# Kernel tuning notes

Hardware: AMD Instinct MI355X
Metric: run time of the kernel (lower is better)

Reference implementation:

```python
import jax, jax.numpy as jnp
import numpy as np

N_WORD_IDS, N_TAG_IDS, N_DEPREL_IDS = 100000, 48, 40
N_WORD_F, N_TAG_F, N_DEPREL_F = 18, 18, 12
EMBED, HIDDEN, N_CLASSES = 128, 1024, 3
B = 16384
N_TOTAL = N_WORD_F + N_TAG_F + N_DEPREL_F  # 48


def _he(key, shape):
    fan_in = shape[0]
    return jax.random.normal(key, shape, dtype=jnp.float32) * jnp.sqrt(2.0 / fan_in)


def setup_inputs() -> dict:
    key = jax.random.key(0)
    ks = jax.random.split(key, 8)
    return {
        "word_id_batch": jax.random.randint(ks[0], (B, N_WORD_F), 0, N_WORD_IDS, dtype=jnp.int64 if jax.config.jax_enable_x64 else jnp.int32).astype(jnp.int32),
        "tag_id_batch": jax.random.randint(ks[1], (B, N_TAG_F), 0, N_TAG_IDS).astype(jnp.int32),
        "deprel_id_batch": jax.random.randint(ks[2], (B, N_DEPREL_F), 0, N_DEPREL_IDS).astype(jnp.int32),
        "word_embeddings": jax.random.normal(ks[3], (N_WORD_IDS, EMBED), dtype=jnp.float32) * 0.1,
        "tag_embeddings": _he(ks[4], (N_TAG_IDS, EMBED)),
        "deprel_embeddings": _he(ks[5], (N_DEPREL_IDS, EMBED)),
        "W_h": _he(ks[6], (N_TOTAL * EMBED, HIDDEN)),
        "b_h": jnp.zeros((HIDDEN,), jnp.float32),
        "W_o": _he(ks[7], (HIDDEN, N_CLASSES)),
        "b_o": jnp.zeros((N_CLASSES,), jnp.float32),
    }


def reference(word_id_batch, tag_id_batch, deprel_id_batch,
              word_embeddings, tag_embeddings, deprel_embeddings,
              W_h, b_h, W_o, b_o):
    # one_hot_float(ids) @ E is mathematically a row gather: E[ids]
    b = word_id_batch.shape[0]
    x = jnp.concatenate([
        word_embeddings[word_id_batch].reshape(b, -1),      # (B, 18*E)
        tag_embeddings[tag_id_batch].reshape(b, -1),        # (B, 18*E)
        deprel_embeddings[deprel_id_batch].reshape(b, -1),  # (B, 12*E)
    ], axis=1)                                              # (B, 48*E)
    h = jax.nn.relu(x @ W_h + b_h)
    # dropout is identity in eval mode (self.training == False)
    return h @ W_o + b_o
```

## Files before the change

kernel.cpp:

```cpp
#include <hip/hip_runtime.h>
#include <hip/hip_bf16.h>
#include <cstdint>

typedef unsigned short u16;
typedef __attribute__((ext_vector_type(8))) short bf16x8;
typedef __attribute__((ext_vector_type(4))) float f32x4;

#define B_ROWS 16384
#define N_HID  1024
#define K_DIM  6144
#define EMB    128
#define N_WORD 100000
#define N_TAG  48
#define N_DEP  40

__device__ __forceinline__ u16 f2bf(float x) {
  union { float f; uint32_t u; } v; v.f = x;
  uint32_t r = v.u + 0x7fffu + ((v.u >> 16) & 1u);
  return (u16)(r >> 16);
}

__device__ __forceinline__ void gload_lds16(const void* g, void* l) {
  __builtin_amdgcn_global_load_lds(
      (const __attribute__((address_space(1))) void*)g,
      (__attribute__((address_space(3))) void*)l, 16, 0, 0);
}

__global__ void init_out_kernel(float* __restrict__ out, const float* __restrict__ b_o) {
  int i = blockIdx.x * blockDim.x + threadIdx.x;
  if (i < B_ROWS * 3) out[i] = b_o[i % 3];
}

__global__ void transpose_wh_kernel(const float* __restrict__ Wh, u16* __restrict__ Wt) {
  __shared__ float tile[32][33];
  int k0 = blockIdx.x * 32, n0 = blockIdx.y * 32;
  int tx = threadIdx.x & 31, ty = threadIdx.x >> 5;
  #pragma unroll
  for (int j = 0; j < 4; ++j)
    tile[ty + j * 8][tx] = Wh[(size_t)(k0 + ty + j * 8) * N_HID + n0 + tx];
  __syncthreads();
  #pragma unroll
  for (int j = 0; j < 4; ++j)
    Wt[(size_t)(n0 + ty + j * 8) * K_DIM + k0 + tx] = f2bf(tile[tx][ty + j * 8]);
}

__global__ void cast_tables_kernel(const float* __restrict__ wordE, const float* __restrict__ tagE,
                                   const float* __restrict__ depE, u16* __restrict__ wordB,
                                   u16* __restrict__ tagB, u16* __restrict__ depB) {
  const int W8 = N_WORD * EMB / 8, T8 = N_TAG * EMB / 8, D8 = N_DEP * EMB / 8;
  int i = blockIdx.x * blockDim.x + threadIdx.x;
  const float* src; u16* dst; int j;
  if (i < W8)            { src = wordE; dst = wordB; j = i; }
  else if (i < W8 + T8)  { src = tagE;  dst = tagB;  j = i - W8; }
  else if (i < W8 + T8 + D8) { src = depE; dst = depB; j = i - W8 - T8; }
  else return;
  const float4* s = (const float4*)(src + (size_t)j * 8);
  float4 v0 = s[0], v1 = s[1];
  bf16x8 w;
  w[0] = (short)f2bf(v0.x); w[1] = (short)f2bf(v0.y);
  w[2] = (short)f2bf(v0.z); w[3] = (short)f2bf(v0.w);
  w[4] = (short)f2bf(v1.x); w[5] = (short)f2bf(v1.y);
  w[6] = (short)f2bf(v1.z); w[7] = (short)f2bf(v1.w);
  *(bf16x8*)(dst + (size_t)j * 8) = w;
}

__global__ __launch_bounds__(256, 4) void fused_v2_kernel(
    const int* __restrict__ word_ids, const int* __restrict__ tag_ids,
    const int* __restrict__ dep_ids,  const u16* __restrict__ wordB,
    const u16* __restrict__ tagB,     const u16* __restrict__ depB,
    const u16* __restrict__ Wt,       const float* __restrict__ b_h,
    const float* __restrict__ W_o,    float* __restrict__ out) {
  __shared__ u16 As[128 * 64];
  __shared__ u16 Bs[128 * 64];

  const int tid  = threadIdx.x;
  const int lane = tid & 63;
  const int wid  = tid >> 6;
  const int wr   = wid >> 1, wc = wid & 1;
  const int bm0  = blockIdx.y * 128;
  const int bn0  = blockIdx.x * 128;

  f32x4 acc[4][4] = {};

  for (int kt = 0; kt < K_DIM / 64; ++kt) {
    __syncthreads();
    {
      int f = kt >> 1, e0 = (kt & 1) << 6;
      const int* ids; const u16* tbl; int nf, fl;
      if (f < 18)      { ids = word_ids; tbl = wordB; nf = 18; fl = f; }
      else if (f < 36) { ids = tag_ids;  tbl = tagB;  nf = 18; fl = f - 18; }
      else             { ids = dep_ids;  tbl = depB;  nf = 12; fl = f - 36; }
      #pragma unroll
      for (int it = 0; it < 4; ++it) {
        int cidx = wid * 256 + it * 64 + lane;
        int r = cidx >> 3, c = cidx & 7;
        int id = ids[(bm0 + r) * nf + fl];
        const u16* src = tbl + (size_t)id * EMB + e0 + ((c ^ (r & 7)) << 3);
        gload_lds16(src, &As[(wid * 256 + it * 64) * 8]);
      }
    }
    #pragma unroll
    for (int it = 0; it < 4; ++it) {
      int cidx = wid * 256 + it * 64 + lane;
      int rn = cidx >> 3, c = cidx & 7;
      const u16* src = Wt + (size_t)(bn0 + rn) * K_DIM + kt * 64 + ((c ^ (rn & 7)) << 3);
      gload_lds16(src, &Bs[(wid * 256 + it * 64) * 8]);
    }
    __syncthreads();
    const int l15 = lane & 15, ca = lane >> 4;
    #pragma unroll
    for (int ks = 0; ks < 2; ++ks) {
      bf16x8 a[4], b[4];
      #pragma unroll
      for (int m = 0; m < 4; ++m) {
        int ra = wr * 64 + m * 16 + l15;
        int ch = (ca + ks * 4) ^ (ra & 7);
        a[m] = *(const bf16x8*)&As[ra * 64 + ch * 8];
      }
      #pragma unroll
      for (int n = 0; n < 4; ++n) {
        int rb = wc * 64 + n * 16 + l15;
        int ch = (ca + ks * 4) ^ (rb & 7);
        b[n] = *(const bf16x8*)&Bs[rb * 64 + ch * 8];
      }
      #pragma unroll
      for (int m = 0; m < 4; ++m)
        #pragma unroll
        for (int n = 0; n < 4; ++n)
          acc[m][n] = __builtin_amdgcn_mfma_f32_16x16x32_bf16(a[m], b[n], acc[m][n], 0, 0, 0);
    }
  }

  float bh[4], wo[4][3];
  #pragma unroll
  for (int n = 0; n < 4; ++n) {
    int j = bn0 + wc * 64 + n * 16 + (lane & 15);
    bh[n] = b_h[j];
    wo[n][0] = W_o[j * 3 + 0]; wo[n][1] = W_o[j * 3 + 1]; wo[n][2] = W_o[j * 3 + 2];
  }
  #pragma unroll
  for (int m = 0; m < 4; ++m) {
    #pragma unroll
    for (int reg = 0; reg < 4; ++reg) {
      float p0 = 0.f, p1 = 0.f, p2 = 0.f;
      #pragma unroll
      for (int n = 0; n < 4; ++n) {
        float h = acc[m][n][reg] + bh[n];
        h = fmaxf(h, 0.f);
        p0 += h * wo[n][0]; p1 += h * wo[n][1]; p2 += h * wo[n][2];
      }
      #pragma unroll
      for (int mask = 1; mask < 16; mask <<= 1) {
        p0 += __shfl_xor(p0, mask);
        p1 += __shfl_xor(p1, mask);
        p2 += __shfl_xor(p2, mask);
      }
      if ((lane & 15) == 0) {
        int row = bm0 + wr * 64 + m * 16 + ((lane >> 4) << 2) + reg;
        atomicAdd(&out[row * 3 + 0], p0);
        atomicAdd(&out[row * 3 + 1], p1);
        atomicAdd(&out[row * 3 + 2], p2);
      }
    }
  }
}

template <bool USE_WT>
__global__ __launch_bounds__(256, 2) void fused_parser_kernel(
    const int* __restrict__ word_ids, const int* __restrict__ tag_ids,
    const int* __restrict__ dep_ids,  const float* __restrict__ wordE,
    const float* __restrict__ tagE,   const float* __restrict__ depE,
    const float* __restrict__ Wh,     const u16* __restrict__ Wt,
    const float* __restrict__ b_h,    const float* __restrict__ W_o,
    float* __restrict__ out) {
  __shared__ u16 As[128 * 72];
  __shared__ u16 Bs[128 * 72];
  const int tid  = threadIdx.x;
  const int lane = tid & 63;
  const int wid  = tid >> 6;
  const int wr   = wid >> 1, wc = wid & 1;
  const int bm0  = blockIdx.y * 128;
  const int bn0  = blockIdx.x * 128;
  f32x4 acc[4][4] = {};
  const int r    = tid & 127;
  const int half = tid >> 7;

  for (int kt = 0; kt < K_DIM / 64; ++kt) {
    __syncthreads();
    {
      int f  = kt >> 1;
      int e0 = (kt & 1) << 6;
      int brow = bm0 + r;
      int id; const float* table;
      if (f < 18)      { id = word_ids[brow * 18 + f];        table = wordE; }
      else if (f < 36) { id = tag_ids[brow * 18 + (f - 18)];  table = tagE;  }
      else             { id = dep_ids[brow * 12 + (f - 36)];  table = depE;  }
      const float4* src = (const float4*)(table + (size_t)id * EMB + e0 + half * 32);
      u16* dst = &As[r * 72 + half * 32];
      #pragma unroll
      for (int j = 0; j < 4; ++j) {
        float4 v0 = src[2 * j], v1 = src[2 * j + 1];
        bf16x8 w;
        w[0] = (short)f2bf(v0.x); w[1] = (short)f2bf(v0.y);
        w[2] = (short)f2bf(v0.z); w[3] = (short)f2bf(v0.w);
        w[4] = (short)f2bf(v1.x); w[5] = (short)f2bf(v1.y);
        w[6] = (short)f2bf(v1.z); w[7] = (short)f2bf(v1.w);
        *(bf16x8*)(dst + j * 8) = w;
      }
    }
    if (USE_WT) {
      const bf16x8* src = (const bf16x8*)(Wt + (size_t)(bn0 + r) * K_DIM + kt * 64 + half * 32);
      u16* dst = &Bs[r * 72 + half * 32];
      #pragma unroll
      for (int j = 0; j < 4; ++j) *(bf16x8*)(dst + j * 8) = src[j];
    } else {
      int kk = tid >> 2, q = tid & 3;
      const float4* src = (const float4*)(Wh + (size_t)(kt * 64 + kk) * N_HID + bn0 + q * 32);
      #pragma unroll
      for (int j = 0; j < 8; ++j) {
        float4 v = src[j];
        int nb = q * 32 + j * 4;
        Bs[(nb + 0) * 72 + kk] = f2bf(v.x);
        Bs[(nb + 1) * 72 + kk] = f2bf(v.y);
        Bs[(nb + 2) * 72 + kk] = f2bf(v.z);
        Bs[(nb + 3) * 72 + kk] = f2bf(v.w);
      }
    }
    __syncthreads();
    const u16* pa = &As[(wr * 64 + (lane & 15)) * 72 + ((lane >> 4) * 8)];
    const u16* pb = &Bs[(wc * 64 + (lane & 15)) * 72 + ((lane >> 4) * 8)];
    #pragma unroll
    for (int ks = 0; ks < 2; ++ks) {
      bf16x8 a[4], b[4];
      #pragma unroll
      for (int m = 0; m < 4; ++m) a[m] = *(const bf16x8*)(pa + m * 16 * 72 + ks * 32);
      #pragma unroll
      for (int n = 0; n < 4; ++n) b[n] = *(const bf16x8*)(pb + n * 16 * 72 + ks * 32);
      #pragma unroll
      for (int m = 0; m < 4; ++m)
        #pragma unroll
        for (int n = 0; n < 4; ++n)
          acc[m][n] = __builtin_amdgcn_mfma_f32_16x16x32_bf16(a[m], b[n], acc[m][n], 0, 0, 0);
    }
  }

  float bh[4], wo[4][3];
  #pragma unroll
  for (int n = 0; n < 4; ++n) {
    int j = bn0 + wc * 64 + n * 16 + (lane & 15);
    bh[n] = b_h[j];
    wo[n][0] = W_o[j * 3 + 0]; wo[n][1] = W_o[j * 3 + 1]; wo[n][2] = W_o[j * 3 + 2];
  }
  #pragma unroll
  for (int m = 0; m < 4; ++m) {
    #pragma unroll
    for (int reg = 0; reg < 4; ++reg) {
      float p0 = 0.f, p1 = 0.f, p2 = 0.f;
      #pragma unroll
      for (int n = 0; n < 4; ++n) {
        float h = acc[m][n][reg] + bh[n];
        h = fmaxf(h, 0.f);
        p0 += h * wo[n][0]; p1 += h * wo[n][1]; p2 += h * wo[n][2];
      }
      #pragma unroll
      for (int mask = 1; mask < 16; mask <<= 1) {
        p0 += __shfl_xor(p0, mask);
        p1 += __shfl_xor(p1, mask);
        p2 += __shfl_xor(p2, mask);
      }
      if ((lane & 15) == 0) {
        int row = bm0 + wr * 64 + m * 16 + ((lane >> 4) << 2) + reg;
        atomicAdd(&out[row * 3 + 0], p0);
        atomicAdd(&out[row * 3 + 1], p1);
        atomicAdd(&out[row * 3 + 2], p2);
      }
    }
  }
}

extern "C" void kernel_launch(void* const* d_in, const int* in_sizes, int n_in,
                              void* d_out, int out_size, void* d_ws, size_t ws_size,
                              hipStream_t stream) {
  const int*   word_ids = (const int*)d_in[0];
  const int*   tag_ids  = (const int*)d_in[1];
  const int*   dep_ids  = (const int*)d_in[2];
  const float* wordE    = (const float*)d_in[3];
  const float* tagE     = (const float*)d_in[4];
  const float* depE     = (const float*)d_in[5];
  const float* Wh       = (const float*)d_in[6];
  const float* b_h      = (const float*)d_in[7];
  const float* W_o      = (const float*)d_in[8];
  const float* b_o      = (const float*)d_in[9];
  float*       out      = (float*)d_out;

  const size_t WT_ELEMS   = (size_t)N_HID * K_DIM;
  const size_t WORD_ELEMS = (size_t)N_WORD * EMB;
  const size_t TAG_ELEMS  = (size_t)N_TAG * EMB;
  const size_t DEP_ELEMS  = (size_t)N_DEP * EMB;
  const size_t NEED_V2 = (WT_ELEMS + WORD_ELEMS + TAG_ELEMS + DEP_ELEMS) * sizeof(u16);
  const size_t NEED_WT = WT_ELEMS * sizeof(u16);

  u16* Wt    = (u16*)d_ws;
  u16* wordB = Wt + WT_ELEMS;
  u16* tagB  = wordB + WORD_ELEMS;
  u16* depB  = tagB + TAG_ELEMS;

  init_out_kernel<<<(B_ROWS * 3 + 255) / 256, 256, 0, stream>>>(out, b_o);

  dim3 grid(N_HID / 128, B_ROWS / 128);
  if (d_ws && ws_size >= NEED_V2) {
    transpose_wh_kernel<<<dim3(K_DIM / 32, N_HID / 32), 256, 0, stream>>>(Wh, Wt);
    const int CAST8 = (int)((WORD_ELEMS + TAG_ELEMS + DEP_ELEMS) / 8);
    cast_tables_kernel<<<(CAST8 + 255) / 256, 256, 0, stream>>>(wordE, tagE, depE, wordB, tagB, depB);
    fused_v2_kernel<<<grid, 256, 0, stream>>>(
        word_ids, tag_ids, dep_ids, wordB, tagB, depB, Wt, b_h, W_o, out);
  } else if (d_ws && ws_size >= NEED_WT) {
    transpose_wh_kernel<<<dim3(K_DIM / 32, N_HID / 32), 256, 0, stream>>>(Wh, Wt);
    fused_parser_kernel<true><<<grid, 256, 0, stream>>>(
        word_ids, tag_ids, dep_ids, wordE, tagE, depE, Wh, Wt, b_h, W_o, out);
  } else {
    fused_parser_kernel<false><<<grid, 256, 0, stream>>>(
        word_ids, tag_ids, dep_ids, wordE, tagE, depE, Wh, Wt, b_h, W_o, out);
  }
}
```

Measured before the change: 345.4 us.

## Add 256x256 double-buffered pipelined GEMM with precomputed gather offsets

Adds a new main kernel with 256x256 tiles and 512 threads. Shared-memory A and B tiles are double-buffered, and global-to-LDS loads are interleaved with MFMA phases using explicit waitcnt, sched barriers and setprio. A pre-pass turns the word/tag/deprel ids into flat offsets into one merged bf16 table, which removes per-tile id lookups and branches. The aim is to hide gather and weight load latency and to get more reuse per tile. The costs are an extra pre-pass kernel, more workspace, and fewer resident blocks because of the larger LDS footprint. The old fp32-fallback path is dropped.

```diff
diff --git a/kernel.cpp b/kernel.cpp
--- a/kernel.cpp
+++ b/kernel.cpp
@@ -13,6 +13,8 @@
 #define N_WORD 100000
 #define N_TAG  48
 #define N_DEP  40
+#define NTILES 96
+#define NITER  48
 
 __device__ __forceinline__ u16 f2bf(float x) {
   union { float f; uint32_t u; } v; v.f = x;
@@ -26,6 +28,14 @@
       (__attribute__((address_space(3))) void*)l, 16, 0, 0);
 }
 
+#define SBAR do { \
+  __builtin_amdgcn_sched_barrier(0); \
+  asm volatile("" ::: "memory"); \
+  __builtin_amdgcn_s_barrier(); \
+  asm volatile("" ::: "memory"); \
+  __builtin_amdgcn_sched_barrier(0); \
+} while (0)
+
 __global__ void init_out_kernel(float* __restrict__ out, const float* __restrict__ b_o) {
   int i = blockIdx.x * blockDim.x + threadIdx.x;
   if (i < B_ROWS * 3) out[i] = b_o[i % 3];
@@ -45,14 +55,13 @@
 }
 
 __global__ void cast_tables_kernel(const float* __restrict__ wordE, const float* __restrict__ tagE,
-                                   const float* __restrict__ depE, u16* __restrict__ wordB,
-                                   u16* __restrict__ tagB, u16* __restrict__ depB) {
+                                   const float* __restrict__ depE, u16* __restrict__ tblB) {
   const int W8 = N_WORD * EMB / 8, T8 = N_TAG * EMB / 8, D8 = N_DEP * EMB / 8;
   int i = blockIdx.x * blockDim.x + threadIdx.x;
-  const float* src; u16* dst; int j;
-  if (i < W8)            { src = wordE; dst = wordB; j = i; }
-  else if (i < W8 + T8)  { src = tagE;  dst = tagB;  j = i - W8; }
-  else if (i < W8 + T8 + D8) { src = depE; dst = depB; j = i - W8 - T8; }
+  const float* src; int j;
+  if (i < W8)                { src = wordE; j = i; }
+  else if (i < W8 + T8)      { src = tagE;  j = i - W8; }
+  else if (i < W8 + T8 + D8) { src = depE;  j = i - W8 - T8; }
   else return;
   const float4* s = (const float4*)(src + (size_t)j * 8);
   float4 v0 = s[0], v1 = s[1];
@@ -61,93 +70,164 @@
   w[2] = (short)f2bf(v0.z); w[3] = (short)f2bf(v0.w);
   w[4] = (short)f2bf(v1.x); w[5] = (short)f2bf(v1.y);
   w[6] = (short)f2bf(v1.z); w[7] = (short)f2bf(v1.w);
-  *(bf16x8*)(dst + (size_t)j * 8) = w;
-}
-
-__global__ __launch_bounds__(256, 4) void fused_v2_kernel(
-    const int* __restrict__ word_ids, const int* __restrict__ tag_ids,
-    const int* __restrict__ dep_ids,  const u16* __restrict__ wordB,
-    const u16* __restrict__ tagB,     const u16* __restrict__ depB,
-    const u16* __restrict__ Wt,       const float* __restrict__ b_h,
-    const float* __restrict__ W_o,    float* __restrict__ out) {
-  __shared__ u16 As[128 * 64];
-  __shared__ u16 Bs[128 * 64];
+  *(bf16x8*)(tblB + (size_t)i * 8) = w;
+}
+
+__global__ void build_offv_kernel(const int* __restrict__ w, const int* __restrict__ t,
+                                  const int* __restrict__ d, int* __restrict__ offv) {
+  int row = blockIdx.x * 256 + threadIdx.x;
+  int f = blockIdx.y;
+  if (row >= B_ROWS) return;
+  int off;
+  if (f < 18)      off = w[row * 18 + f] * EMB;
+  else if (f < 36) off = N_WORD * EMB + t[row * 18 + (f - 18)] * EMB;
+  else             off = (N_WORD + N_TAG) * EMB + d[row * 12 + (f - 36)] * EMB;
+  offv[f * B_ROWS + row] = off;
+}
+
+__device__ __forceinline__ void rd_b4(const u16* base, int sch, bf16x8* q) {
+  #pragma unroll
+  for (int nf = 0; nf < 4; ++nf) q[nf] = *(const bf16x8*)(base + nf * 1024 + sch);
+}
+__device__ __forceinline__ void rd_a4(const u16* base, int sch, int mh, bf16x8* q) {
+  #pragma unroll
+  for (int mf = 0; mf < 4; ++mf) q[mf] = *(const bf16x8*)(base + (mh * 4 + mf) * 1024 + sch);
+}
+__device__ __forceinline__ void mfma16(f32x4 (&acc)[8][4], int mh, const bf16x8* aT, const bf16x8* bq) {
+  #pragma unroll
+  for (int m = 0; m < 4; ++m)
+    #pragma unroll
+    for (int n = 0; n < 4; ++n)
+      acc[mh * 4 + m][n] = __builtin_amdgcn_mfma_f32_16x16x32_bf16(aT[m], bq[n], acc[mh * 4 + m][n], 0, 0, 0);
+}
+
+__global__ __launch_bounds__(512, 2) void fused_v3_kernel(
+    const u16* __restrict__ tblB, const int* __restrict__ offv,
+    const u16* __restrict__ Wt,   const float* __restrict__ b_h,
+    const float* __restrict__ W_o, float* __restrict__ out) {
+  __shared__ u16 As[2][256 * 64];
+  __shared__ u16 Bs[2][256 * 64];
 
   const int tid  = threadIdx.x;
   const int lane = tid & 63;
   const int wid  = tid >> 6;
-  const int wr   = wid >> 1, wc = wid & 1;
-  const int bm0  = blockIdx.y * 128;
-  const int bn0  = blockIdx.x * 128;
-
-  f32x4 acc[4][4] = {};
-
-  for (int kt = 0; kt < K_DIM / 64; ++kt) {
-    __syncthreads();
-    {
-      int f = kt >> 1, e0 = (kt & 1) << 6;
-      const int* ids; const u16* tbl; int nf, fl;
-      if (f < 18)      { ids = word_ids; tbl = wordB; nf = 18; fl = f; }
-      else if (f < 36) { ids = tag_ids;  tbl = tagB;  nf = 18; fl = f - 18; }
-      else             { ids = dep_ids;  tbl = depB;  nf = 12; fl = f - 36; }
-      #pragma unroll
-      for (int it = 0; it < 4; ++it) {
-        int cidx = wid * 256 + it * 64 + lane;
-        int r = cidx >> 3, c = cidx & 7;
-        int id = ids[(bm0 + r) * nf + fl];
-        const u16* src = tbl + (size_t)id * EMB + e0 + ((c ^ (r & 7)) << 3);
-        gload_lds16(src, &As[(wid * 256 + it * 64) * 8]);
-      }
-    }
-    #pragma unroll
-    for (int it = 0; it < 4; ++it) {
-      int cidx = wid * 256 + it * 64 + lane;
-      int rn = cidx >> 3, c = cidx & 7;
-      const u16* src = Wt + (size_t)(bn0 + rn) * K_DIM + kt * 64 + ((c ^ (rn & 7)) << 3);
-      gload_lds16(src, &Bs[(wid * 256 + it * 64) * 8]);
-    }
-    __syncthreads();
-    const int l15 = lane & 15, ca = lane >> 4;
-    #pragma unroll
-    for (int ks = 0; ks < 2; ++ks) {
-      bf16x8 a[4], b[4];
-      #pragma unroll
-      for (int m = 0; m < 4; ++m) {
-        int ra = wr * 64 + m * 16 + l15;
-        int ch = (ca + ks * 4) ^ (ra & 7);
-        a[m] = *(const bf16x8*)&As[ra * 64 + ch * 8];
-      }
-      #pragma unroll
-      for (int n = 0; n < 4; ++n) {
-        int rb = wc * 64 + n * 16 + l15;
-        int ch = (ca + ks * 4) ^ (rb & 7);
-        b[n] = *(const bf16x8*)&Bs[rb * 64 + ch * 8];
-      }
-      #pragma unroll
-      for (int m = 0; m < 4; ++m)
-        #pragma unroll
-        for (int n = 0; n < 4; ++n)
-          acc[m][n] = __builtin_amdgcn_mfma_f32_16x16x32_bf16(a[m], b[n], acc[m][n], 0, 0, 0);
-    }
+  const int wr   = wid >> 2;
+  const int wc   = wid & 3;
+  const int bn0  = blockIdx.x * 256;
+  const int bm0  = blockIdx.y * 256;
+  const int l15  = lane & 15, ca = lane >> 4;
+
+  const int r0 = tid >> 3;
+  const int c  = tid & 7;
+  const int sc = ((c ^ (r0 & 7)) << 3);
+  const u16* Bp[4];
+  #pragma unroll
+  for (int j = 0; j < 4; ++j)
+    Bp[j] = Wt + (size_t)(bn0 + j * 64 + r0) * K_DIM + sc;
+  const int ivb = bm0 + r0;
+
+#define DESTA(buf, h, is) ((void*)&As[buf][(h) * 8192 + (is) * 4096 + wid * 512])
+#define DESTB(buf, h, is) ((void*)&Bs[buf][(h) * 8192 + (is) * 4096 + wid * 512])
+#define STAGE_B2(buf, h, t) do { \
+    gload_lds16(Bp[2 * (h)] + (size_t)(t) * 64, DESTB(buf, h, 0)); \
+    gload_lds16(Bp[2 * (h) + 1] + (size_t)(t) * 64, DESTB(buf, h, 1)); } while (0)
+#define STAGE_A2(buf, h, e0) do { \
+    gload_lds16(tblB + (size_t)oA[2 * (h)] + (e0) + sc, DESTA(buf, h, 0)); \
+    gload_lds16(tblB + (size_t)oA[2 * (h) + 1] + (e0) + sc, DESTA(buf, h, 1)); } while (0)
+
+  const u16* aBase0 = &As[0][(wr * 128 + l15) * 64];
+  const u16* aBase1 = &As[1][(wr * 128 + l15) * 64];
+  const u16* bBase0 = &Bs[0][(wc * 64 + l15) * 64];
+  const u16* bBase1 = &Bs[1][(wc * 64 + l15) * 64];
+  const int sch0 = ((ca    ) ^ (l15 & 7)) << 3;
+  const int sch1 = ((ca + 4) ^ (l15 & 7)) << 3;
+
+  f32x4 acc[8][4] = {};
+  int oA[4];
+
+  STAGE_B2(0, 0, 0); STAGE_B2(0, 1, 0);
+  #pragma unroll
+  for (int j = 0; j < 4; ++j) oA[j] = offv[ivb + j * 64];
+  STAGE_A2(0, 0, 0); STAGE_A2(0, 1, 0);
+  STAGE_B2(1, 0, 1); STAGE_B2(1, 1, 1);
+  asm volatile("s_waitcnt vmcnt(4)" ::: "memory");
+  SBAR;
+
+  #pragma unroll 1
+  for (int i = 0; i < NITER; ++i) {
+    const int T = 2 * i;
+    bf16x8 bq0[4], bq1[4], aT[4];
+    rd_b4(bBase0, sch0, bq0);
+    rd_a4(aBase0, sch0, 0, aT);
+    STAGE_A2(1, 0, 64);
+    SBAR;
+    __builtin_amdgcn_s_setprio(1); mfma16(acc, 0, aT, bq0); __builtin_amdgcn_s_setprio(0);
+    SBAR;
+    rd_b4(bBase0, sch1, bq1);
+    rd_a4(aBase0, sch0, 1, aT);
+    STAGE_A2(1, 1, 64);
+    SBAR;
+    __builtin_amdgcn_s_setprio(1); mfma16(acc, 1, aT, bq0); __builtin_amdgcn_s_setprio(0);
+    SBAR;
+    if (i + 1 < NITER) {
+      const int* ov = offv + (i + 1) * B_ROWS + ivb;
+      #pragma unroll
+      for (int j = 0; j < 4; ++j) oA[j] = ov[j * 64];
+    }
+    rd_a4(aBase0, sch1, 0, aT);
+    if (T + 2 < NTILES) STAGE_B2(0, 0, T + 2);
+    SBAR;
+    __builtin_amdgcn_s_setprio(1); mfma16(acc, 0, aT, bq1); __builtin_amdgcn_s_setprio(0);
+    SBAR;
+    rd_a4(aBase0, sch1, 1, aT);
+    if (T + 2 < NTILES) STAGE_B2(0, 1, T + 2);
+    if (i == NITER - 1) { asm volatile("s_waitcnt vmcnt(0)" ::: "memory"); }
+    else                { asm volatile("s_waitcnt vmcnt(8)" ::: "memory"); }
+    SBAR;
+    __builtin_amdgcn_s_setprio(1); mfma16(acc, 1, aT, bq1); __builtin_amdgcn_s_setprio(0);
+    SBAR;
+    rd_b4(bBase1, sch0, bq0);
+    rd_a4(aBase1, sch0, 0, aT);
+    if (T + 2 < NTILES) STAGE_A2(0, 0, 0);
+    SBAR;
+    __builtin_amdgcn_s_setprio(1); mfma16(acc, 0, aT, bq0); __builtin_amdgcn_s_setprio(0);
+    SBAR;
+    rd_b4(bBase1, sch1, bq1);
+    rd_a4(aBase1, sch0, 1, aT);
+    if (T + 2 < NTILES) STAGE_A2(0, 1, 0);
+    SBAR;
+    __builtin_amdgcn_s_setprio(1); mfma16(acc, 1, aT, bq0); __builtin_amdgcn_s_setprio(0);
+    SBAR;
+    rd_a4(aBase1, sch1, 0, aT);
+    if (T + 3 < NTILES) STAGE_B2(1, 0, T + 3);
+    SBAR;
+    __builtin_amdgcn_s_setprio(1); mfma16(acc, 0, aT, bq1); __builtin_amdgcn_s_setprio(0);
+    SBAR;
+    rd_a4(aBase1, sch1, 1, aT);
+    if (T + 3 < NTILES) STAGE_B2(1, 1, T + 3);
+    asm volatile("s_waitcnt vmcnt(4)" ::: "memory");
+    SBAR;
+    __builtin_amdgcn_s_setprio(1); mfma16(acc, 1, aT, bq1); __builtin_amdgcn_s_setprio(0);
+    SBAR;
   }
 
   float bh[4], wo[4][3];
   #pragma unroll
-  for (int n = 0; n < 4; ++n) {
-    int j = bn0 + wc * 64 + n * 16 + (lane & 15);
-    bh[n] = b_h[j];
-    wo[n][0] = W_o[j * 3 + 0]; wo[n][1] = W_o[j * 3 + 1]; wo[n][2] = W_o[j * 3 + 2];
-  }
-  #pragma unroll
-  for (int m = 0; m < 4; ++m) {
+  for (int nf = 0; nf < 4; ++nf) {
+    int j = bn0 + wc * 64 + nf * 16 + l15;
+    bh[nf] = b_h[j];
+    wo[nf][0] = W_o[j * 3 + 0]; wo[nf][1] = W_o[j * 3 + 1]; wo[nf][2] = W_o[j * 3 + 2];
+  }
+  #pragma unroll
+  for (int mf = 0; mf < 8; ++mf) {
     #pragma unroll
     for (int reg = 0; reg < 4; ++reg) {
       float p0 = 0.f, p1 = 0.f, p2 = 0.f;
       #pragma unroll
-      for (int n = 0; n < 4; ++n) {
-        float h = acc[m][n][reg] + bh[n];
+      for (int nf = 0; nf < 4; ++nf) {
+        float h = acc[mf][nf][reg] + bh[nf];
         h = fmaxf(h, 0.f);
-        p0 += h * wo[n][0]; p1 += h * wo[n][1]; p2 += h * wo[n][2];
+        p0 += h * wo[nf][0]; p1 += h * wo[nf][1]; p2 += h * wo[nf][2];
       }
       #pragma unroll
       for (int mask = 1; mask < 16; mask <<= 1) {
@@ -155,26 +235,27 @@
         p1 += __shfl_xor(p1, mask);
         p2 += __shfl_xor(p2, mask);
       }
-      if ((lane & 15) == 0) {
-        int row = bm0 + wr * 64 + m * 16 + ((lane >> 4) << 2) + reg;
+      if (l15 == 0) {
+        int row = bm0 + wr * 128 + mf * 16 + (ca << 2) + reg;
         atomicAdd(&out[row * 3 + 0], p0);
         atomicAdd(&out[row * 3 + 1], p1);
         atomicAdd(&out[row * 3 + 2], p2);
       }
     }
   }
-}
-
-template <bool USE_WT>
-__global__ __launch_bounds__(256, 2) void fused_parser_kernel(
+#undef DESTA
+#undef DESTB
+#undef STAGE_B2
+#undef STAGE_A2
+}
+
+__global__ __launch_bounds__(256, 4) void fused_v2_kernel(
     const int* __restrict__ word_ids, const int* __restrict__ tag_ids,
-    const int* __restrict__ dep_ids,  const float* __restrict__ wordE,
-    const float* __restrict__ tagE,   const float* __restrict__ depE,
-    const float* __restrict__ Wh,     const u16* __restrict__ Wt,
-    const float* __restrict__ b_h,    const float* __restrict__ W_o,
-    float* __restrict__ out) {
-  __shared__ u16 As[128 * 72];
-  __shared__ u16 Bs[128 * 72];
+    const int* __restrict__ dep_ids,  const u16* __restrict__ tblB,
+    const u16* __restrict__ Wt,       const float* __restrict__ b_h,
+    const float* __restrict__ W_o,    float* __restrict__ out) {
+  __shared__ u16 As2[128 * 64];
+  __shared__ u16 Bs2[128 * 64];
   const int tid  = threadIdx.x;
   const int lane = tid & 63;
   const int wid  = tid >> 6;
@@ -182,60 +263,48 @@
   const int bm0  = blockIdx.y * 128;
   const int bn0  = blockIdx.x * 128;
   f32x4 acc[4][4] = {};
-  const int r    = tid & 127;
-  const int half = tid >> 7;
 
   for (int kt = 0; kt < K_DIM / 64; ++kt) {
     __syncthreads();
     {
-      int f  = kt >> 1;
-      int e0 = (kt & 1) << 6;
-      int brow = bm0 + r;
-      int id; const float* table;
-      if (f < 18)      { id = word_ids[brow * 18 + f];        table = wordE; }
-      else if (f < 36) { id = tag_ids[brow * 18 + (f - 18)];  table = tagE;  }
-      else             { id = dep_ids[brow * 12 + (f - 36)];  table = depE;  }
-      const float4* src = (const float4*)(table + (size_t)id * EMB + e0 + half * 32);
-      u16* dst = &As[r * 72 + half * 32];
-      #pragma unroll
-      for (int j = 0; j < 4; ++j) {
-        float4 v0 = src[2 * j], v1 = src[2 * j + 1];
-        bf16x8 w;
-        w[0] = (short)f2bf(v0.x); w[1] = (short)f2bf(v0.y);
-        w[2] = (short)f2bf(v0.z); w[3] = (short)f2bf(v0.w);
-        w[4] = (short)f2bf(v1.x); w[5] = (short)f2bf(v1.y);
-        w[6] = (short)f2bf(v1.z); w[7] = (short)f2bf(v1.w);
-        *(bf16x8*)(dst + j * 8) = w;
-      }
-    }
-    if (USE_WT) {
-      const bf16x8* src = (const bf16x8*)(Wt + (size_t)(bn0 + r) * K_DIM + kt * 64 + half * 32);
-      u16* dst = &Bs[r * 72 + half * 32];
-      #pragma unroll
-      for (int j = 0; j < 4; ++j) *(bf16x8*)(dst + j * 8) = src[j];
-    } else {
-      int kk = tid >> 2, q = tid & 3;
-      const float4* src = (const float4*)(Wh + (size_t)(kt * 64 + kk) * N_HID + bn0 + q * 32);
-      #pragma unroll
-      for (int j = 0; j < 8; ++j) {
-        float4 v = src[j];
-        int nb = q * 32 + j * 4;
-        Bs[(nb + 0) * 72 + kk] = f2bf(v.x);
-        Bs[(nb + 1) * 72 + kk] = f2bf(v.y);
-        Bs[(nb + 2) * 72 + kk] = f2bf(v.z);
-        Bs[(nb + 3) * 72 + kk] = f2bf(v.w);
-      }
+      int f = kt >> 1, e0 = (kt & 1) << 6;
+      const int* ids; int nf, fl; size_t tb;
+      if (f < 18)      { ids = word_ids; nf = 18; fl = f;      tb = 0; }
+      else if (f < 36) { ids = tag_ids;  nf = 18; fl = f - 18; tb = (size_t)N_WORD * EMB; }
+      else             { ids = dep_ids;  nf = 12; fl = f - 36; tb = (size_t)(N_WORD + N_TAG) * EMB; }
+      #pragma unroll
+      for (int it = 0; it < 4; ++it) {
+        int cidx = wid * 256 + it * 64 + lane;
+        int r = cidx >> 3, cc = cidx & 7;
+        int id = ids[(bm0 + r) * nf + fl];
+        const u16* src = tblB + tb + (size_t)id * EMB + e0 + ((cc ^ (r & 7)) << 3);
+        gload_lds16(src, &As2[(wid * 256 + it * 64) * 8]);
+      }
+    }
+    #pragma unroll
+    for (int it = 0; it < 4; ++it) {
+      int cidx = wid * 256 + it * 64 + lane;
+      int rn = cidx >> 3, cc = cidx & 7;
+      const u16* src = Wt + (size_t)(bn0 + rn) * K_DIM + kt * 64 + ((cc ^ (rn & 7)) << 3);
+      gload_lds16(src, &Bs2[(wid * 256 + it * 64) * 8]);
     }
     __syncthreads();
-    const u16* pa = &As[(wr * 64 + (lane & 15)) * 72 + ((lane >> 4) * 8)];
-    const u16* pb = &Bs[(wc * 64 + (lane & 15)) * 72 + ((lane >> 4) * 8)];
+    const int l15 = lane & 15, ca = lane >> 4;
     #pragma unroll
     for (int ks = 0; ks < 2; ++ks) {
       bf16x8 a[4], b[4];
       #pragma unroll
-      for (int m = 0; m < 4; ++m) a[m] = *(const bf16x8*)(pa + m * 16 * 72 + ks * 32);
-      #pragma unroll
-      for (int n = 0; n < 4; ++n) b[n] = *(const bf16x8*)(pb + n * 16 * 72 + ks * 32);
+      for (int m = 0; m < 4; ++m) {
+        int ra = wr * 64 + m * 16 + l15;
+        int ch = (ca + ks * 4) ^ (ra & 7);
+        a[m] = *(const bf16x8*)&As2[ra * 64 + ch * 8];
+      }
+      #pragma unroll
+      for (int n = 0; n < 4; ++n) {
+        int rb = wc * 64 + n * 16 + l15;
+        int ch = (ca + ks * 4) ^ (rb & 7);
+        b[n] = *(const bf16x8*)&Bs2[rb * 64 + ch * 8];
+      }
       #pragma unroll
       for (int m = 0; m < 4; ++m)
         #pragma unroll
@@ -244,10 +313,11 @@
     }
   }
 
+  const int l15 = lane & 15;
   float bh[4], wo[4][3];
   #pragma unroll
   for (int n = 0; n < 4; ++n) {
-    int j = bn0 + wc * 64 + n * 16 + (lane & 15);
+    int j = bn0 + wc * 64 + n * 16 + l15;
     bh[n] = b_h[j];
     wo[n][0] = W_o[j * 3 + 0]; wo[n][1] = W_o[j * 3 + 1]; wo[n][2] = W_o[j * 3 + 2];
   }
@@ -268,7 +338,7 @@
         p1 += __shfl_xor(p1, mask);
         p2 += __shfl_xor(p2, mask);
       }
-      if ((lane & 15) == 0) {
+      if (l15 == 0) {
         int row = bm0 + wr * 64 + m * 16 + ((lane >> 4) << 2) + reg;
         atomicAdd(&out[row * 3 + 0], p0);
         atomicAdd(&out[row * 3 + 1], p1);
@@ -293,33 +363,28 @@
   const float* b_o      = (const float*)d_in[9];
   float*       out      = (float*)d_out;
 
-  const size_t WT_ELEMS   = (size_t)N_HID * K_DIM;
-  const size_t WORD_ELEMS = (size_t)N_WORD * EMB;
-  const size_t TAG_ELEMS  = (size_t)N_TAG * EMB;
-  const size_t DEP_ELEMS  = (size_t)N_DEP * EMB;
-  const size_t NEED_V2 = (WT_ELEMS + WORD_ELEMS + TAG_ELEMS + DEP_ELEMS) * sizeof(u16);
-  const size_t NEED_WT = WT_ELEMS * sizeof(u16);
-
-  u16* Wt    = (u16*)d_ws;
-  u16* wordB = Wt + WT_ELEMS;
-  u16* tagB  = wordB + WORD_ELEMS;
-  u16* depB  = tagB + TAG_ELEMS;
+  const size_t WT_ELEMS  = (size_t)N_HID * K_DIM;
+  const size_t TBL_ELEMS = (size_t)(N_WORD + N_TAG + N_DEP) * EMB;
+  const size_t OFFV_ELEMS = (size_t)48 * B_ROWS;
+  const size_t NEED_V2 = (WT_ELEMS + TBL_ELEMS) * sizeof(u16);
+  const size_t NEED_V3 = NEED_V2 + OFFV_ELEMS * sizeof(int);
+
+  u16* Wt   = (u16*)d_ws;
+  u16* tblB = Wt + WT_ELEMS;
+  int* offv = (int*)(tblB + TBL_ELEMS);
 
   init_out_kernel<<<(B_ROWS * 3 + 255) / 256, 256, 0, stream>>>(out, b_o);
 
-  dim3 grid(N_HID / 128, B_ROWS / 128);
-  if (d_ws && ws_size >= NEED_V2) {
+  if (d_ws && ws_size >= NEED_V3) {
     transpose_wh_kernel<<<dim3(K_DIM / 32, N_HID / 32), 256, 0, stream>>>(Wh, Wt);
-    const int CAST8 = (int)((WORD_ELEMS + TAG_ELEMS + DEP_ELEMS) / 8);
-    cast_tables_kernel<<<(CAST8 + 255) / 256, 256, 0, stream>>>(wordE, tagE, depE, wordB, tagB, depB);
-    fused_v2_kernel<<<grid, 256, 0, stream>>>(
-        word_ids, tag_ids, dep_ids, wordB, tagB, depB, Wt, b_h, W_o, out);
-  } else if (d_ws && ws_size >= NEED_WT) {
+    cast_tables_kernel<<<(int)((TBL_ELEMS / 8 + 255) / 256), 256, 0, stream>>>(wordE, tagE, depE, tblB);
+    build_offv_kernel<<<dim3(B_ROWS / 256, 48), 256, 0, stream>>>(word_ids, tag_ids, dep_ids, offv);
+    fused_v3_kernel<<<dim3(N_HID / 256, B_ROWS / 256), 512, 0, stream>>>(
+        tblB, offv, Wt, b_h, W_o, out);
+  } else if (d_ws && ws_size >= NEED_V2) {
     transpose_wh_kernel<<<dim3(K_DIM / 32, N_HID / 32), 256, 0, stream>>>(Wh, Wt);
-    fused_parser_kernel<true><<<grid, 256, 0, stream>>>(
-        word_ids, tag_ids, dep_ids, wordE, tagE, depE, Wh, Wt, b_h, W_o, out);
-  } else {
-    fused_parser_kernel<false><<<grid, 256, 0, stream>>>(
-        word_ids, tag_ids, dep_ids, wordE, tagE, depE, Wh, Wt, b_h, W_o, out);
-  }
-}
+    cast_tables_kernel<<<(int)((TBL_ELEMS / 8 + 255) / 256), 256, 0, stream>>>(wordE, tagE, depE, tblB);
+    fused_v2_kernel<<<dim3(N_HID / 128, B_ROWS / 128), 256, 0, stream>>>(
+        word_ids, tag_ids, dep_ids, tblB, Wt, b_h, W_o, out);
+  }
+}
```

After: 325.1 us. 5.9% less time.
